# Optimization experiments

Measured on AMD Instinct MI355X. Metric: run time of the kernel, lower is better.

The kernel has to match this reference:

```python
import jax, jax.numpy as jnp
import numpy as np

B, L, D_MODEL, H, D_QKV = 4, 2048, 1024, 16, 64
SCALE = float(D_MODEL) ** 0.5  # note: source scales by sqrt(d_model), not sqrt(d_qkv)


def setup_inputs() -> dict:
    key = jax.random.key(0)
    ks = jax.random.split(key, 6)
    xavier_qkv = (2.0 / (D_MODEL + D_QKV)) ** 0.5
    xavier_fc = (2.0 / (H * D_QKV + D_MODEL)) ** 0.5
    return {
        "x": jax.random.normal(ks[0], (B, L, D_MODEL), dtype=jnp.float32),
        "mask": jnp.ones((B, L), dtype=jnp.int32),
        "w_q": jax.random.normal(ks[1], (H, D_MODEL, D_QKV), dtype=jnp.float32) * xavier_qkv,
        "w_k": jax.random.normal(ks[2], (H, D_MODEL, D_QKV), dtype=jnp.float32) * xavier_qkv,
        "w_v": jax.random.normal(ks[3], (H, D_MODEL, D_QKV), dtype=jnp.float32) * xavier_qkv,
        "fc_w": jax.random.normal(ks[4], (D_MODEL, H * D_QKV), dtype=jnp.float32) * xavier_fc,
        "fc_b": jnp.zeros((D_MODEL,), dtype=jnp.float32),
    }


def reference(x, mask, w_q, w_k, w_v, fc_w, fc_b):
    # x: [B, L, M]; per-head projections via einsum, as in the source
    q = jnp.einsum('blm,hmd->blhd', x, w_q)
    k = jnp.einsum('blm,hmd->blhd', x, w_k)
    v = jnp.einsum('blm,hmd->blhd', x, w_v)
    scores = jnp.einsum('blhd,bkhd->bhlk', q, k)  # [B, H, L, L]
    m = mask[:, None, None, :]  # unsqueeze(1).unsqueeze(2)
    scores = jnp.where(m == 0, jnp.asarray(-1e9, scores.dtype), scores)
    logits = jax.nn.softmax(scores / SCALE, axis=3)
    # Faithful to source einsum 'bhlk,blhd->blhd' (k is summed out of logits only)
    out = jnp.einsum('bhlk,blhd->blhd', logits, v)
    out = out.reshape(x.shape[0], x.shape[1], H * D_QKV)
    return out @ fc_w.T + fc_b
```

## Files before the change

kernel.cpp:

```cpp
#include <hip/hip_runtime.h>
#include <hip/hip_bf16.h>


typedef __attribute__((ext_vector_type(8))) short bf16x8;
typedef __attribute__((ext_vector_type(4))) float f32x4;

__device__ __forceinline__ f32x4 mfma16(bf16x8 a, bf16x8 b, f32x4 c) {
  return __builtin_amdgcn_mfma_f32_16x16x32_bf16(a, b, c, 0, 0, 0);
}

__device__ __forceinline__ unsigned short f2b(float f) {
  unsigned int u = __builtin_bit_cast(unsigned int, f);
  return (unsigned short)((u + 0x7fffu + ((u >> 16) & 1u)) >> 16);
}

__device__ __forceinline__ bf16x8 cvt8(float4 a, float4 b) {
  bf16x8 r;
  r[0] = (short)f2b(a.x); r[1] = (short)f2b(a.y); r[2] = (short)f2b(a.z); r[3] = (short)f2b(a.w);
  r[4] = (short)f2b(b.x); r[5] = (short)f2b(b.y); r[6] = (short)f2b(b.z); r[7] = (short)f2b(b.w);
  return r;
}

__device__ __forceinline__ void gld_lds16(const void* g, void* l) {
  __builtin_amdgcn_global_load_lds((const __attribute__((address_space(1))) unsigned int*)g,
                                   (__attribute__((address_space(3))) unsigned int*)l, 16, 0, 0);
}

__global__ __launch_bounds__(256) void prep(const float* __restrict__ x,
                                            const float* __restrict__ wv,
                                            const float* __restrict__ fcw,
                                            unsigned short* __restrict__ xb,
                                            unsigned short* __restrict__ wcT) {
  __shared__ __align__(16) short As[2][64 * 64];
  __shared__ __align__(16) short Bs[2][64 * 64];

  int bid = blockIdx.x, t = threadIdx.x;
  int wid = t >> 6, lane = t & 63, l16 = lane & 15, quad = lane >> 4;

  if (bid < 256) {
    int j0 = (bid >> 4) * 64;
    int m0 = (bid & 15) * 64;
    int wr = wid >> 1, wc = wid & 1;
    int rowt = t >> 3, colb = (t & 7) * 8;

    f32x4 acc[2][2];
#pragma unroll
    for (int a = 0; a < 2; a++)
#pragma unroll
      for (int b = 0; b < 2; b++) acc[a][b] = (f32x4){0.f, 0.f, 0.f, 0.f};

    float4 ra0[2][2], rb0[2][2], ra1[2][2], rb1[2][2];

#define LOADH(h, ra, rb)                                                             \
    {                                                                                \
      _Pragma("unroll")                                                              \
      for (int c = 0; c < 2; c++) {                                                  \
        int row = c * 32 + rowt;                                                     \
        const float* pa = fcw + (j0 + row) * 1024 + (h) * 64 + colb;                 \
        ra[c][0] = *reinterpret_cast<const float4*>(pa);                             \
        ra[c][1] = *reinterpret_cast<const float4*>(pa + 4);                         \
        const float* pb = wv + (h) * 65536 + (m0 + row) * 64 + colb;                 \
        rb[c][0] = *reinterpret_cast<const float4*>(pb);                             \
        rb[c][1] = *reinterpret_cast<const float4*>(pb + 4);                         \
      }                                                                              \
    }
#define STOREH(buf, ra, rb)                                                          \
    {                                                                                \
      _Pragma("unroll")                                                              \
      for (int c = 0; c < 2; c++) {                                                  \
        int row = c * 32 + rowt;                                                     \
        int bo = row * 128 + ((colb * 2) ^ ((row & 7) << 4));                        \
        *reinterpret_cast<bf16x8*>((char*)As[buf] + bo) = cvt8(ra[c][0], ra[c][1]);  \
        *reinterpret_cast<bf16x8*>((char*)Bs[buf] + bo) = cvt8(rb[c][0], rb[c][1]);  \
      }                                                                              \
    }
#define COMPUTE_FOLD(buf)                                                            \
    {                                                                                \
      bf16x8 af[2][2], bg[2][2];                                                     \
      _Pragma("unroll")                                                              \
      for (int rt = 0; rt < 2; rt++) {                                               \
        int rowf = wr * 32 + rt * 16 + l16;                                          \
        int rbase = rowf * 128, rx = (rowf & 7) << 4;                                \
        af[rt][0] = *reinterpret_cast<const bf16x8*>((char*)As[buf] + rbase + ((quad * 16) ^ rx));        \
        af[rt][1] = *reinterpret_cast<const bf16x8*>((char*)As[buf] + rbase + ((64 + quad * 16) ^ rx));   \
      }                                                                              \
      _Pragma("unroll")                                                              \
      for (int ct = 0; ct < 2; ct++) {                                               \
        int rowf = wc * 32 + ct * 16 + l16;                                          \
        int rbase = rowf * 128, rx = (rowf & 7) << 4;                                \
        bg[ct][0] = *reinterpret_cast<const bf16x8*>((char*)Bs[buf] + rbase + ((quad * 16) ^ rx));        \
        bg[ct][1] = *reinterpret_cast<const bf16x8*>((char*)Bs[buf] + rbase + ((64 + quad * 16) ^ rx));   \
      }                                                                              \
      _Pragma("unroll")                                                              \
      for (int ks = 0; ks < 2; ks++)                                                 \
        _Pragma("unroll")                                                            \
        for (int rt = 0; rt < 2; rt++)                                               \
          _Pragma("unroll")                                                          \
          for (int ct = 0; ct < 2; ct++)                                             \
            acc[rt][ct] = mfma16(af[rt][ks], bg[ct][ks], acc[rt][ct]);               \
    }

    LOADH(0, ra0, rb0);
    LOADH(1, ra1, rb1);
    STOREH(0, ra0, rb0);
    __syncthreads();

    for (int hh = 0; hh < 16; hh += 2) {
      if (hh < 14) LOADH(hh + 2, ra0, rb0);
      COMPUTE_FOLD(0);
      STOREH(1, ra1, rb1);
      __syncthreads();

      if (hh < 13) LOADH(hh + 3, ra1, rb1);
      COMPUTE_FOLD(1);
      if (hh < 14) STOREH(0, ra0, rb0);
      __syncthreads();
    }
#undef LOADH
#undef STOREH
#undef COMPUTE_FOLD

#pragma unroll
    for (int rt = 0; rt < 2; rt++)
#pragma unroll
      for (int ct = 0; ct < 2; ct++) {
        int jj = j0 + wr * 32 + rt * 16 + quad * 4;
        int mm = m0 + wc * 32 + ct * 16 + l16;
#pragma unroll
        for (int r = 0; r < 4; r++) wcT[(jj + r) * 1024 + mm] = f2b(acc[rt][ct][r]);
      }
  } else {
    int cb = bid - 256;
    for (int ch = cb; ch < 4096; ch += 768) {
      int idx = ch * 2048 + t * 8;
      float4 a = *reinterpret_cast<const float4*>(x + idx);
      float4 b = *reinterpret_cast<const float4*>(x + idx + 4);
      *reinterpret_cast<bf16x8*>(xb + idx) = cvt8(a, b);
    }
  }
}

__global__ __launch_bounds__(256, 2) void final_gemm(const unsigned short* __restrict__ xb,
                                                     const unsigned short* __restrict__ wcT,
                                                     const float* __restrict__ fcb,
                                                     float* __restrict__ out) {
  __shared__ __align__(16) unsigned short As[2 * 128 * 32];
  __shared__ __align__(16) unsigned short Bs[2 * 128 * 32];
  int t = threadIdx.x, wid = t >> 6, lane = t & 63, l16 = lane & 15, quad = lane >> 4;
  int wr = wid >> 1, wc = wid & 1;
  int swz = (blockIdx.x & 7) * 64 + (blockIdx.x >> 3);
  int row0 = (swz >> 3) * 128;
  int col0 = (swz & 7) * 128;

  int w4 = wid * 4;
  const unsigned short* Ap[4];
  const unsigned short* Bp[4];
#pragma unroll
  for (int j = 0; j < 4; j++) {
    int blk = w4 + j, s = blk >> 3;
    int row = (blk & 7) * 16 + (lane >> 2), kq = lane & 3;
    Ap[j] = xb + (row0 + row) * 1024 + s * 32 + kq * 8;
    Bp[j] = wcT + (col0 + row) * 1024 + s * 32 + kq * 8;
  }

  f32x4 acc[4][4];
#pragma unroll
  for (int rt = 0; rt < 4; rt++)
#pragma unroll
    for (int ct = 0; ct < 4; ct++) acc[rt][ct] = (f32x4){0.f, 0.f, 0.f, 0.f};

  for (int k0 = 0; k0 < 1024; k0 += 64) {
    __syncthreads();
#pragma unroll
    for (int j = 0; j < 4; j++) {
      gld_lds16(Ap[j] + k0, &As[(w4 + j) * 512 + lane * 8]);
      gld_lds16(Bp[j] + k0, &Bs[(w4 + j) * 512 + lane * 8]);
    }
    __syncthreads();
#pragma unroll
    for (int s = 0; s < 2; s++) {
      bf16x8 af[4], bfr[4];
#pragma unroll
      for (int rt = 0; rt < 4; rt++)
        af[rt] = *reinterpret_cast<const bf16x8*>(&As[s * 4096 + (wr * 64 + rt * 16 + l16) * 32 + quad * 8]);
#pragma unroll
      for (int ct = 0; ct < 4; ct++)
        bfr[ct] = *reinterpret_cast<const bf16x8*>(&Bs[s * 4096 + (wc * 64 + ct * 16 + l16) * 32 + quad * 8]);
#pragma unroll
      for (int rt = 0; rt < 4; rt++)
#pragma unroll
        for (int ct = 0; ct < 4; ct++)
          acc[rt][ct] = mfma16(af[rt], bfr[ct], acc[rt][ct]);
    }
  }

#pragma unroll
  for (int ct = 0; ct < 4; ct++) {
    int j = col0 + wc * 64 + ct * 16 + l16;
    float bias = fcb[j];
#pragma unroll
    for (int rt = 0; rt < 4; rt++) {
      int i0 = row0 + wr * 64 + rt * 16 + quad * 4;
      f32x4 a = acc[rt][ct];
#pragma unroll
      for (int r = 0; r < 4; r++) out[(i0 + r) * 1024 + j] = a[r] + bias;
    }
  }
}

extern "C" void kernel_launch(void* const* d_in, const int* in_sizes, int n_in,
                              void* d_out, int out_size, void* d_ws, size_t ws_size,
                              hipStream_t stream) {
  const float* x   = (const float*)d_in[0];
  const float* wv  = (const float*)d_in[4];
  const float* fcw = (const float*)d_in[5];
  const float* fcb = (const float*)d_in[6];
  float* out = (float*)d_out;

  char* ws = (char*)d_ws;
  unsigned short* xb  = (unsigned short*)(ws);
  unsigned short* wcT = (unsigned short*)(ws + 16777216);

  prep<<<1024, 256, 0, stream>>>(x, wv, fcw, xb, wcT);
  final_gemm<<<512, 256, 0, stream>>>(xb, wcT, fcb, out);
}
```

Before: 127.9 us.

## Fuse fp32-to-bf16 conversion of x into final GEMM load path

The separate pass that converts x to bf16 in the prep kernel is removed. The final GEMM now loads fp32 x directly into registers, converts it, and stores bf16 into LDS, while the weight operand still uses direct global-to-LDS loads. This avoids writing and re-reading a 16 MB bf16 copy of x, but each GEMM block re-reads its fp32 A tile, eight times across column blocks, which doubles the bytes per read. The prep grid is also trimmed to the fold blocks, with an XCD-aware block-to-tile mapping.

```diff
diff --git a/kernel.cpp b/kernel.cpp
--- a/kernel.cpp
+++ b/kernel.cpp
@@ -26,10 +26,8 @@
                                    (__attribute__((address_space(3))) unsigned int*)l, 16, 0, 0);
 }
 
-__global__ __launch_bounds__(256) void prep(const float* __restrict__ x,
-                                            const float* __restrict__ wv,
+__global__ __launch_bounds__(256) void prep(const float* __restrict__ wv,
                                             const float* __restrict__ fcw,
-                                            unsigned short* __restrict__ xb,
                                             unsigned short* __restrict__ wcT) {
   __shared__ __align__(16) short As[2][64 * 64];
   __shared__ __align__(16) short Bs[2][64 * 64];
@@ -37,19 +35,19 @@
   int bid = blockIdx.x, t = threadIdx.x;
   int wid = t >> 6, lane = t & 63, l16 = lane & 15, quad = lane >> 4;
 
-  if (bid < 256) {
-    int j0 = (bid >> 4) * 64;
-    int m0 = (bid & 15) * 64;
-    int wr = wid >> 1, wc = wid & 1;
-    int rowt = t >> 3, colb = (t & 7) * 8;
-
-    f32x4 acc[2][2];
-#pragma unroll
-    for (int a = 0; a < 2; a++)
-#pragma unroll
-      for (int b = 0; b < 2; b++) acc[a][b] = (f32x4){0.f, 0.f, 0.f, 0.f};
-
-    float4 ra0[2][2], rb0[2][2], ra1[2][2], rb1[2][2];
+  int xcd = bid & 7, idx = bid >> 3;
+  int j0 = (xcd * 2 + (idx & 1)) * 64;
+  int m0 = (idx >> 1) * 64;
+  int wr = wid >> 1, wc = wid & 1;
+  int rowt = t >> 3, colb = (t & 7) * 8;
+
+  f32x4 acc[2][2];
+#pragma unroll
+  for (int a = 0; a < 2; a++)
+#pragma unroll
+    for (int b = 0; b < 2; b++) acc[a][b] = (f32x4){0.f, 0.f, 0.f, 0.f};
+
+  float4 ra0[2][2], rb0[2][2], ra1[2][2], rb1[2][2];
 
 #define LOADH(h, ra, rb)                                                             \
     {                                                                                \
@@ -100,47 +98,38 @@
             acc[rt][ct] = mfma16(af[rt][ks], bg[ct][ks], acc[rt][ct]);               \
     }
 
-    LOADH(0, ra0, rb0);
-    LOADH(1, ra1, rb1);
-    STOREH(0, ra0, rb0);
-    __syncthreads();
-
-    for (int hh = 0; hh < 16; hh += 2) {
-      if (hh < 14) LOADH(hh + 2, ra0, rb0);
-      COMPUTE_FOLD(0);
-      STOREH(1, ra1, rb1);
-      __syncthreads();
-
-      if (hh < 13) LOADH(hh + 3, ra1, rb1);
-      COMPUTE_FOLD(1);
-      if (hh < 14) STOREH(0, ra0, rb0);
-      __syncthreads();
-    }
+  LOADH(0, ra0, rb0);
+  LOADH(1, ra1, rb1);
+  STOREH(0, ra0, rb0);
+  __syncthreads();
+
+  for (int hh = 0; hh < 16; hh += 2) {
+    if (hh < 14) LOADH(hh + 2, ra0, rb0);
+    COMPUTE_FOLD(0);
+    STOREH(1, ra1, rb1);
+    __syncthreads();
+
+    if (hh < 13) LOADH(hh + 3, ra1, rb1);
+    COMPUTE_FOLD(1);
+    if (hh < 14) STOREH(0, ra0, rb0);
+    __syncthreads();
+  }
 #undef LOADH
 #undef STOREH
 #undef COMPUTE_FOLD
 
 #pragma unroll
-    for (int rt = 0; rt < 2; rt++)
-#pragma unroll
-      for (int ct = 0; ct < 2; ct++) {
-        int jj = j0 + wr * 32 + rt * 16 + quad * 4;
-        int mm = m0 + wc * 32 + ct * 16 + l16;
-#pragma unroll
-        for (int r = 0; r < 4; r++) wcT[(jj + r) * 1024 + mm] = f2b(acc[rt][ct][r]);
-      }
-  } else {
-    int cb = bid - 256;
-    for (int ch = cb; ch < 4096; ch += 768) {
-      int idx = ch * 2048 + t * 8;
-      float4 a = *reinterpret_cast<const float4*>(x + idx);
-      float4 b = *reinterpret_cast<const float4*>(x + idx + 4);
-      *reinterpret_cast<bf16x8*>(xb + idx) = cvt8(a, b);
-    }
-  }
-}
-
-__global__ __launch_bounds__(256, 2) void final_gemm(const unsigned short* __restrict__ xb,
+  for (int rt = 0; rt < 2; rt++)
+#pragma unroll
+    for (int ct = 0; ct < 2; ct++) {
+      int jj = j0 + wr * 32 + rt * 16 + quad * 4;
+      int mm = m0 + wc * 32 + ct * 16 + l16;
+#pragma unroll
+      for (int r = 0; r < 4; r++) wcT[(jj + r) * 1024 + mm] = f2b(acc[rt][ct][r]);
+    }
+}
+
+__global__ __launch_bounds__(256, 2) void final_gemm(const float* __restrict__ x,
                                                      const unsigned short* __restrict__ wcT,
                                                      const float* __restrict__ fcb,
                                                      float* __restrict__ out) {
@@ -153,13 +142,13 @@
   int col0 = (swz & 7) * 128;
 
   int w4 = wid * 4;
-  const unsigned short* Ap[4];
+  const float* Axp[4];
   const unsigned short* Bp[4];
 #pragma unroll
   for (int j = 0; j < 4; j++) {
     int blk = w4 + j, s = blk >> 3;
     int row = (blk & 7) * 16 + (lane >> 2), kq = lane & 3;
-    Ap[j] = xb + (row0 + row) * 1024 + s * 32 + kq * 8;
+    Axp[j] = x + (row0 + row) * 1024 + s * 32 + kq * 8;
     Bp[j] = wcT + (col0 + row) * 1024 + s * 32 + kq * 8;
   }
 
@@ -171,11 +160,17 @@
 
   for (int k0 = 0; k0 < 1024; k0 += 64) {
     __syncthreads();
+    float4 av[4][2];
 #pragma unroll
     for (int j = 0; j < 4; j++) {
-      gld_lds16(Ap[j] + k0, &As[(w4 + j) * 512 + lane * 8]);
-      gld_lds16(Bp[j] + k0, &Bs[(w4 + j) * 512 + lane * 8]);
-    }
+      av[j][0] = *reinterpret_cast<const float4*>(Axp[j] + k0);
+      av[j][1] = *reinterpret_cast<const float4*>(Axp[j] + k0 + 4);
+    }
+#pragma unroll
+    for (int j = 0; j < 4; j++) gld_lds16(Bp[j] + k0, &Bs[(w4 + j) * 512 + lane * 8]);
+#pragma unroll
+    for (int j = 0; j < 4; j++)
+      *reinterpret_cast<bf16x8*>(&As[(w4 + j) * 512 + lane * 8]) = cvt8(av[j][0], av[j][1]);
     __syncthreads();
 #pragma unroll
     for (int s = 0; s < 2; s++) {
@@ -217,10 +212,8 @@
   const float* fcb = (const float*)d_in[6];
   float* out = (float*)d_out;
 
-  char* ws = (char*)d_ws;
-  unsigned short* xb  = (unsigned short*)(ws);
-  unsigned short* wcT = (unsigned short*)(ws + 16777216);
-
-  prep<<<1024, 256, 0, stream>>>(x, wv, fcw, xb, wcT);
-  final_gemm<<<512, 256, 0, stream>>>(xb, wcT, fcb, out);
-}
+  unsigned short* wcT = (unsigned short*)d_ws;
+
+  prep<<<256, 256, 0, stream>>>(wv, fcw, wcT);
+  final_gemm<<<512, 256, 0, stream>>>(x, wcT, fcb, out);
+}
```

After: 141.9 us. 11.0% more time.
